# Performance work log

Hardware: AMD Instinct MI355X
Metric: run time of the kernel (lower is better)

The kernel has to match this reference:

```python
import jax, jax.numpy as jnp
import numpy as np

NTOKENS = 6144
SPLIT = 2048          # splits = [0, 2048, inf]
TEMP = 65.0
N, D = 128, 256


def setup_inputs() -> dict:
    key = jax.random.key(0)
    k1, k2, k3, k4, k5, k6 = jax.random.split(key, 6)
    hiddens = jax.random.normal(k1, (N, D), dtype=jnp.float32)
    targets = jax.random.randint(k2, (N,), 0, NTOKENS)
    emb = jax.random.normal(k3, (NTOKENS + 1, D), dtype=jnp.float32)  # +1 tail-target token
    W = jax.random.normal(k4, (D, D), dtype=jnp.float32) / np.sqrt(D)
    U = jax.random.normal(k5, (D, D), dtype=jnp.float32) / np.sqrt(D)
    b = jax.random.normal(k6, (D,), dtype=jnp.float32)
    return {"hiddens": hiddens, "targets": targets, "emb": emb, "W": W, "U": U, "b": b}


def _logprob(h, words_emb, W, U, b):
    # h: [N, d]; words_emb: [V, d]
    # surrogate one-step RNN-cell model: out = tanh(E[w] @ W + h @ U + b) -> [N, V, d]
    out = jnp.tanh(words_emb @ W + (h @ U + b)[:, None, :])
    # SimpleEuclDistance: squared euclidean distance per (hidden, word)
    dist = jnp.sum((h[:, None, :] - out) ** 2, axis=-1)          # [N, V]
    # SimplePolynomialKernel: k(d) = 1 / (1 + d), scaled by temp
    k = TEMP / (1.0 + dist)
    return jax.nn.log_softmax(k, axis=-1)


def reference(hiddens, targets, emb, W, U, b):
    n_head = SPLIT            # head words 0..SPLIT-1
    n_tail = NTOKENS - SPLIT  # tail words SPLIT..NTOKENS-1
    # head vocab = head words + the single tail-target token (index NTOKENS)
    head_ids = jnp.concatenate([jnp.arange(n_head), jnp.array([NTOKENS])])
    lp_head = _logprob(hiddens, emb[head_ids], W, U, b)          # [N, n_head+1]
    lp_tail = _logprob(hiddens, emb[SPLIT:NTOKENS], W, U, b)     # [N, n_tail]

    is_head = targets < SPLIT
    head_idx = jnp.clip(targets, 0, n_head - 1)
    tail_idx = jnp.clip(targets - SPLIT, 0, n_tail - 1)
    head_loss = -jnp.take_along_axis(lp_head, head_idx[:, None], axis=1)[:, 0]
    # for tail tokens: head part is the tail-target column (last col, softmaxed_head_res[:, -1])
    tail_loss = -(lp_head[:, -1] + jnp.take_along_axis(lp_tail, tail_idx[:, None], axis=1)[:, 0])
    per_token = jnp.where(is_head, head_loss, tail_loss)
    return jnp.sum(per_token) / targets.shape[0]
```

## Files before the change

kernel.cpp:

```cpp
#include <hip/hip_runtime.h>
#include <hip/hip_bf16.h>
#include <cfloat>

#define V_ALL  6145
#define NTOK   6144
#define SPLIT_ 2048
#define NROW   128
#define DDIM   256
#define TEMP_  65.0f
#define C2     2.8853900817779268f

#define EW_OFF 0
#define EW_SZ  (V_ALL * DDIM)
#define HU_OFF (EW_OFF + EW_SZ)
#define HU_SZ  (NROW * DDIM)
#define HS_OFF (HU_OFF + HU_SZ)
#define TS_OFF (HS_OFF + NROW)
#define KT_OFF (TS_OFF + NROW)
#define KL_OFF (KT_OFF + NROW)

__global__ __launch_bounds__(256) void k_hu(const float* __restrict__ h,
                                            const float* __restrict__ U,
                                            const float* __restrict__ b,
                                            float* __restrict__ hUs,
                                            float* __restrict__ hsum,
                                            float* __restrict__ tsum) {
    const int d = threadIdx.x;
    const int n = blockIdx.x;
    if (d == 0) hsum[n] = 0.f;
    if (d == 1) tsum[n] = 0.f;
    const float4* __restrict__ hr = (const float4*)(h + n * DDIM);
    float acc = b[d];
    #pragma unroll 8
    for (int k4 = 0; k4 < DDIM / 4; ++k4) {
        float4 hv = hr[k4];
        int k = k4 * 4;
        acc = fmaf(hv.x, U[(k + 0) * DDIM + d], acc);
        acc = fmaf(hv.y, U[(k + 1) * DDIM + d], acc);
        acc = fmaf(hv.z, U[(k + 2) * DDIM + d], acc);
        acc = fmaf(hv.w, U[(k + 3) * DDIM + d], acc);
    }
    hUs[n * DDIM + d] = C2 * acc;
}

__global__ __launch_bounds__(256) void k_ew(const float* __restrict__ emb,
                                            const float* __restrict__ W,
                                            float* __restrict__ EWs) {
    const int d = threadIdx.x;
    const int v0 = blockIdx.x * 8;
    const float4* __restrict__ er[8];
    #pragma unroll
    for (int i = 0; i < 8; ++i) {
        int r = v0 + i;
        if (r > V_ALL - 1) r = V_ALL - 1;
        er[i] = (const float4*)(emb + r * DDIM);
    }
    float acc[8];
    #pragma unroll
    for (int i = 0; i < 8; ++i) acc[i] = 0.f;

    for (int k4 = 0; k4 < DDIM / 4; ++k4) {
        const int k = k4 * 4;
        const float w0 = W[(k + 0) * DDIM + d];
        const float w1 = W[(k + 1) * DDIM + d];
        const float w2 = W[(k + 2) * DDIM + d];
        const float w3 = W[(k + 3) * DDIM + d];
        #pragma unroll
        for (int i = 0; i < 8; ++i) {
            float4 e = er[i][k4];
            acc[i] = fmaf(e.x, w0, acc[i]);
            acc[i] = fmaf(e.y, w1, acc[i]);
            acc[i] = fmaf(e.z, w2, acc[i]);
            acc[i] = fmaf(e.w, w3, acc[i]);
        }
    }
    #pragma unroll
    for (int i = 0; i < 8; ++i) {
        int r = v0 + i;
        if (r <= V_ALL - 1) EWs[r * DDIM + d] = C2 * acc[i];
    }
}

__global__ __launch_bounds__(256) void k_dist(const float* __restrict__ EWs,
                                              const float* __restrict__ hUs,
                                              const float* __restrict__ h,
                                              const int* __restrict__ targets,
                                              float* __restrict__ hsum,
                                              float* __restrict__ tsum,
                                              float* __restrict__ ktarget,
                                              float* __restrict__ ktail) {
    __shared__ float sEW[16][260];
    __shared__ float sHU[16][260];
    __shared__ float sH [16][260];

    const int v0 = blockIdx.x * 16;
    const int n0 = blockIdx.y * 16;

    #pragma unroll
    for (int j = 0; j < 4; ++j) {
        int idx = threadIdx.x + 256 * j;
        int r   = idx >> 6;
        int c4  = idx & 63;
        int vr  = v0 + r; if (vr > V_ALL - 1) vr = V_ALL - 1;
        *(float4*)&sEW[r][c4 * 4] = *(const float4*)&EWs[vr * DDIM + c4 * 4];
        *(float4*)&sHU[r][c4 * 4] = *(const float4*)&hUs[(n0 + r) * DDIM + c4 * 4];
        *(float4*)&sH [r][c4 * 4] = *(const float4*)&h  [(n0 + r) * DDIM + c4 * 4];
    }
    __syncthreads();

    const int vl = threadIdx.x & 15;
    const int nl = threadIdx.x >> 4;
    const float* pe = &sEW[vl][0];
    const float* pa = &sHU[nl][0];
    const float* ph = &sH [nl][0];

    float acc0 = 0.f, acc1 = 0.f;
    #pragma unroll 4
    for (int d4 = 0; d4 < DDIM / 4; ++d4) {
        float4 e  = *(const float4*)(pe + d4 * 4);
        float4 a  = *(const float4*)(pa + d4 * 4);
        float4 hh = *(const float4*)(ph + d4 * 4);
        { float ex = __builtin_amdgcn_exp2f(e.x + a.x);
          float t  = fmaf(-2.f, __builtin_amdgcn_rcpf(ex + 1.f), 1.f);
          float df = hh.x - t; acc0 = fmaf(df, df, acc0); }
        { float ex = __builtin_amdgcn_exp2f(e.y + a.y);
          float t  = fmaf(-2.f, __builtin_amdgcn_rcpf(ex + 1.f), 1.f);
          float df = hh.y - t; acc1 = fmaf(df, df, acc1); }
        { float ex = __builtin_amdgcn_exp2f(e.z + a.z);
          float t  = fmaf(-2.f, __builtin_amdgcn_rcpf(ex + 1.f), 1.f);
          float df = hh.z - t; acc0 = fmaf(df, df, acc0); }
        { float ex = __builtin_amdgcn_exp2f(e.w + a.w);
          float t  = fmaf(-2.f, __builtin_amdgcn_rcpf(ex + 1.f), 1.f);
          float df = hh.w - t; acc1 = fmaf(df, df, acc1); }
    }
    const float kk = TEMP_ / (1.f + acc0 + acc1);

    const int vg = v0 + vl;
    const int n  = n0 + nl;
    const bool valid = (vg <= NTOK);
    float ek = valid ? __expf(kk - 65.f) : 0.f;

    ek += __shfl_xor(ek, 1, 16);
    ek += __shfl_xor(ek, 2, 16);
    ek += __shfl_xor(ek, 4, 16);
    ek += __shfl_xor(ek, 8, 16);

    const bool is_head = (v0 < SPLIT_) || (v0 >= NTOK);
    if (vl == 0) {
        float* dst = is_head ? hsum : tsum;
        atomicAdd(&dst[n], ek);
    }
    if (valid) {
        int tn = targets[n];
        if (vg == tn)   ktarget[n] = kk;
        if (vg == NTOK) ktail[n]   = kk;
    }
}

__global__ __launch_bounds__(128) void k_loss(const float* __restrict__ hsum,
                                              const float* __restrict__ tsum,
                                              const float* __restrict__ ktarget,
                                              const float* __restrict__ ktail,
                                              const int* __restrict__ targets,
                                              float* __restrict__ out) {
    const int n = threadIdx.x;
    const float logZh = 65.f + logf(hsum[n]);
    const int t = targets[n];
    float loss;
    if (t < SPLIT_) loss = logZh - ktarget[n];
    else            loss = logZh + 65.f + logf(tsum[n]) - ktail[n] - ktarget[n];

    #pragma unroll
    for (int o = 32; o; o >>= 1) loss += __shfl_down(loss, o);
    __shared__ float s[2];
    if ((n & 63) == 0) s[n >> 6] = loss;
    __syncthreads();
    if (n == 0) out[0] = (s[0] + s[1]) / (float)NROW;
}

extern "C" void kernel_launch(void* const* d_in, const int* in_sizes, int n_in,
                              void* d_out, int out_size, void* d_ws, size_t ws_size,
                              hipStream_t stream) {
    const float* h       = (const float*)d_in[0];
    const int*   targets = (const int*)  d_in[1];
    const float* emb     = (const float*)d_in[2];
    const float* W       = (const float*)d_in[3];
    const float* U       = (const float*)d_in[4];
    const float* b       = (const float*)d_in[5];

    float* ws  = (float*)d_ws;
    float* EWs = ws + EW_OFF;
    float* hUs = ws + HU_OFF;
    float* hs  = ws + HS_OFF;
    float* ts  = ws + TS_OFF;
    float* kt  = ws + KT_OFF;
    float* kl  = ws + KL_OFF;

    k_hu  <<<dim3(NROW),   dim3(256), 0, stream>>>(h, U, b, hUs, hs, ts);
    k_ew  <<<dim3(769),    dim3(256), 0, stream>>>(emb, W, EWs);
    k_dist<<<dim3(385, 8), dim3(256), 0, stream>>>(EWs, hUs, h, targets,
                                                   hs, ts, kt, kl);
    k_loss<<<dim3(1),      dim3(128), 0, stream>>>(hs, ts, kt, kl, targets,
                                                   (float*)d_out);
}
```

Baseline: 181.5 us.

## Keep hidden slices in registers and split the distance across lanes in k_dist

k_dist drops its shared-memory staging of EW, hU and h tiles. Each thread now holds a 16-element slice of one hidden row's h and hU in registers and loops over 16 vocabulary rows, reading EW straight from global memory. Partial distances are reduced with 16-lane shuffles, and each row's exp-sums are accumulated before a single atomic. The aim is to remove the heavy LDS traffic (three float4 reads per four transcendentals) and the barrier, at the cost of extra shuffles and per-row division/exp work. In the last block it also reads EW rows past the vocabulary end, which land in other workspace data and are masked out.

```diff
diff --git a/kernel.cpp b/kernel.cpp
--- a/kernel.cpp
+++ b/kernel.cpp
@@ -89,72 +89,60 @@
                                               float* __restrict__ tsum,
                                               float* __restrict__ ktarget,
                                               float* __restrict__ ktail) {
-    __shared__ float sEW[16][260];
-    __shared__ float sHU[16][260];
-    __shared__ float sH [16][260];
+    const int dq = threadIdx.x & 15;
+    const int nl = threadIdx.x >> 4;
+    const int n  = blockIdx.y * 16 + nl;
+    const int v0 = blockIdx.x * 16;
+    const int d0 = dq * 16;
 
-    const int v0 = blockIdx.x * 16;
-    const int n0 = blockIdx.y * 16;
-
+    float4 hr[4], ar[4];
     #pragma unroll
     for (int j = 0; j < 4; ++j) {
-        int idx = threadIdx.x + 256 * j;
-        int r   = idx >> 6;
-        int c4  = idx & 63;
-        int vr  = v0 + r; if (vr > V_ALL - 1) vr = V_ALL - 1;
-        *(float4*)&sEW[r][c4 * 4] = *(const float4*)&EWs[vr * DDIM + c4 * 4];
-        *(float4*)&sHU[r][c4 * 4] = *(const float4*)&hUs[(n0 + r) * DDIM + c4 * 4];
-        *(float4*)&sH [r][c4 * 4] = *(const float4*)&h  [(n0 + r) * DDIM + c4 * 4];
+        hr[j] = *(const float4*)&h  [n * DDIM + d0 + 4 * j];
+        ar[j] = *(const float4*)&hUs[n * DDIM + d0 + 4 * j];
     }
-    __syncthreads();
+    const int tgt = targets[n];
 
-    const int vl = threadIdx.x & 15;
-    const int nl = threadIdx.x >> 4;
-    const float* pe = &sEW[vl][0];
-    const float* pa = &sHU[nl][0];
-    const float* ph = &sH [nl][0];
-
-    float acc0 = 0.f, acc1 = 0.f;
+    float acc_ek = 0.f;
     #pragma unroll 4
-    for (int d4 = 0; d4 < DDIM / 4; ++d4) {
-        float4 e  = *(const float4*)(pe + d4 * 4);
-        float4 a  = *(const float4*)(pa + d4 * 4);
-        float4 hh = *(const float4*)(ph + d4 * 4);
-        { float ex = __builtin_amdgcn_exp2f(e.x + a.x);
-          float t  = fmaf(-2.f, __builtin_amdgcn_rcpf(ex + 1.f), 1.f);
-          float df = hh.x - t; acc0 = fmaf(df, df, acc0); }
-        { float ex = __builtin_amdgcn_exp2f(e.y + a.y);
-          float t  = fmaf(-2.f, __builtin_amdgcn_rcpf(ex + 1.f), 1.f);
-          float df = hh.y - t; acc1 = fmaf(df, df, acc1); }
-        { float ex = __builtin_amdgcn_exp2f(e.z + a.z);
-          float t  = fmaf(-2.f, __builtin_amdgcn_rcpf(ex + 1.f), 1.f);
-          float df = hh.z - t; acc0 = fmaf(df, df, acc0); }
-        { float ex = __builtin_amdgcn_exp2f(e.w + a.w);
-          float t  = fmaf(-2.f, __builtin_amdgcn_rcpf(ex + 1.f), 1.f);
-          float df = hh.w - t; acc1 = fmaf(df, df, acc1); }
+    for (int vi = 0; vi < 16; ++vi) {
+        const int vg = v0 + vi;
+        const float* __restrict__ ep = &EWs[vg * DDIM + d0];
+        float acc0 = 0.f, acc1 = 0.f;
+        #pragma unroll
+        for (int j = 0; j < 4; ++j) {
+            float4 e  = *(const float4*)(ep + 4 * j);
+            float4 a  = ar[j];
+            float4 hh = hr[j];
+            { float E = __builtin_amdgcn_exp2f(e.x + a.x);
+              float t = fmaf(-2.f, __builtin_amdgcn_rcpf(E + 1.f), 1.f);
+              float df = hh.x - t; acc0 = fmaf(df, df, acc0); }
+            { float E = __builtin_amdgcn_exp2f(e.y + a.y);
+              float t = fmaf(-2.f, __builtin_amdgcn_rcpf(E + 1.f), 1.f);
+              float df = hh.y - t; acc1 = fmaf(df, df, acc1); }
+            { float E = __builtin_amdgcn_exp2f(e.z + a.z);
+              float t = fmaf(-2.f, __builtin_amdgcn_rcpf(E + 1.f), 1.f);
+              float df = hh.z - t; acc0 = fmaf(df, df, acc0); }
+            { float E = __builtin_amdgcn_exp2f(e.w + a.w);
+              float t = fmaf(-2.f, __builtin_amdgcn_rcpf(E + 1.f), 1.f);
+              float df = hh.w - t; acc1 = fmaf(df, df, acc1); }
+        }
+        float dist = acc0 + acc1;
+        dist += __shfl_xor(dist, 1, 16);
+        dist += __shfl_xor(dist, 2, 16);
+        dist += __shfl_xor(dist, 4, 16);
+        dist += __shfl_xor(dist, 8, 16);
+        const float kk = TEMP_ / (1.f + dist);
+        float ek = __expf(kk - 65.f);
+        if (vg > NTOK) ek = 0.f;
+        acc_ek += ek;
+        if (dq == 0) {
+            if (vg == tgt)  ktarget[n] = kk;
+            if (vg == NTOK) ktail[n]   = kk;
+        }
     }
-    const float kk = TEMP_ / (1.f + acc0 + acc1);
-
-    const int vg = v0 + vl;
-    const int n  = n0 + nl;
-    const bool valid = (vg <= NTOK);
-    float ek = valid ? __expf(kk - 65.f) : 0.f;
-
-    ek += __shfl_xor(ek, 1, 16);
-    ek += __shfl_xor(ek, 2, 16);
-    ek += __shfl_xor(ek, 4, 16);
-    ek += __shfl_xor(ek, 8, 16);
-
     const bool is_head = (v0 < SPLIT_) || (v0 >= NTOK);
-    if (vl == 0) {
-        float* dst = is_head ? hsum : tsum;
-        atomicAdd(&dst[n], ek);
-    }
-    if (valid) {
-        int tn = targets[n];
-        if (vg == tn)   ktarget[n] = kk;
-        if (vg == NTOK) ktail[n]   = kk;
-    }
+    if (dq == 0) atomicAdd(is_head ? &hsum[n] : &tsum[n], acc_ek);
 }
 
 __global__ __launch_bounds__(128) void k_loss(const float* __restrict__ hsum,
```

Result: slower. 189.8 us (+4.5%).
